# Kernel tuning notes

Hardware: AMD Instinct MI355X
Metric: run time of the kernel (lower is better)

## Reference

```python
import jax, jax.numpy as jnp
import numpy as np

B, S, H = 2, 2048, 2048
NH, NKV, HD = 16, 4, 128  # heads, kv heads, head_dim
GROUP = NH // NKV
THETA = 10000.0
NEG = -1e9


def _rope_tables(seq_len, head_dim, theta):
    inv_freq = 1.0 / (theta ** (jnp.arange(0, head_dim, 2, dtype=jnp.float32) / head_dim))
    t = jnp.arange(seq_len, dtype=jnp.float32)
    freqs = jnp.outer(t, inv_freq)                 # [S, HD/2]
    emb = jnp.concatenate([freqs, freqs], axis=-1)  # [S, HD]
    return jnp.cos(emb), jnp.sin(emb)


def _rotate_half(x):
    half = x.shape[-1] // 2
    return jnp.concatenate([-x[..., half:], x[..., :half]], axis=-1)


def setup_inputs() -> dict:
    key = jax.random.key(0)
    ks = jax.random.split(key, 5)
    scale = 0.02
    x = jax.random.normal(ks[0], (B, S, H), dtype=jnp.float32)
    Wq = jax.random.normal(ks[1], (NH * HD, H), dtype=jnp.float32) * scale
    Wk = jax.random.normal(ks[2], (NKV * HD, H), dtype=jnp.float32) * scale
    Wv = jax.random.normal(ks[3], (NKV * HD, H), dtype=jnp.float32) * scale
    Wo = jax.random.normal(ks[4], (H, NH * HD), dtype=jnp.float32) * scale
    cos, sin = _rope_tables(S, HD, THETA)
    # additive causal mask: 0 on/below diagonal, -1e9 above
    causal = jnp.triu(jnp.full((S, S), NEG, dtype=jnp.float32), k=1)
    mask = causal[None, None]  # [1,1,S,S]
    return {"x": x, "Wq": Wq, "Wk": Wk, "Wv": Wv, "Wo": Wo,
            "cos": cos, "sin": sin, "mask": mask}


def reference(x, Wq, Wk, Wv, Wo, cos, sin, mask):
    b, s, _ = x.shape
    # projections (nn.Linear, no bias): y = x @ W.T
    q = (x @ Wq.T).reshape(b, s, NH, HD).transpose(0, 2, 1, 3)    # [B,NH,S,D]
    k = (x @ Wk.T).reshape(b, s, NKV, HD).transpose(0, 2, 1, 3)   # [B,NKV,S,D]
    v = (x @ Wv.T).reshape(b, s, NKV, HD).transpose(0, 2, 1, 3)   # [B,NKV,S,D]
    # RoPE
    c = cos[None, None]  # [1,1,S,D]
    sn = sin[None, None]
    q = q * c + _rotate_half(q) * sn
    k = k * c + _rotate_half(k) * sn
    # GQA: repeat KV heads to match query heads (mirrors _repeat_kv)
    k = jnp.repeat(k, GROUP, axis=1)  # [B,NH,S,D]
    v = jnp.repeat(v, GROUP, axis=1)
    # scaled dot-product attention with additive mask
    scores = jnp.einsum('bhqd,bhkd->bhqk', q, k) / jnp.sqrt(jnp.float32(HD))
    scores = scores + mask
    p = jax.nn.softmax(scores, axis=-1)
    ctx = jnp.einsum('bhqk,bhkd->bhqd', p, v)            # [B,NH,S,D]
    ctx = ctx.transpose(0, 2, 1, 3).reshape(b, s, NH * HD)
    return ctx @ Wo.T
```

## Files before the change

### kernel.cpp

```cpp
#include <hip/hip_runtime.h>
#include <stdint.h>

#define B_   2
#define S_   2048
#define H_   2048
#define NH_  16
#define NKV_ 4
#define HD_  128
#define M_   (B_ * S_)

typedef short bf16x8 __attribute__((ext_vector_type(8)));
typedef float f32x4  __attribute__((ext_vector_type(4)));

__device__ __forceinline__ float b2f(unsigned short u) {
  union { unsigned int u; float f; } v; v.u = ((unsigned int)u) << 16; return v.f;
}
__device__ __forceinline__ unsigned short f2b(float f) {
  union { float f; unsigned int u; } v; v.f = f;
  unsigned int u = v.u;
  unsigned int r = (u + 0x7FFFu + ((u >> 16) & 1u)) >> 16;
  return (unsigned short)r;
}
__device__ __forceinline__ uint4 pack8(const float4& a, const float4& b) {
  uint4 r;
  r.x = (unsigned)f2b(a.x) | ((unsigned)f2b(a.y) << 16);
  r.y = (unsigned)f2b(a.z) | ((unsigned)f2b(a.w) << 16);
  r.z = (unsigned)f2b(b.x) | ((unsigned)f2b(b.y) << 16);
  r.w = (unsigned)f2b(b.z) | ((unsigned)f2b(b.w) << 16);
  return r;
}
__device__ __forceinline__ void gload_lds(const unsigned short* g, unsigned short* l) {
  __builtin_amdgcn_global_load_lds(
      (const __attribute__((address_space(1))) unsigned int*)g,
      (__attribute__((address_space(3))) unsigned int*)l, 16, 0, 0);
}

__global__ void cvt_bf16(const float* __restrict__ src, unsigned short* __restrict__ dst, int n8)
{
  int i = blockIdx.x * blockDim.x + threadIdx.x;
  if (i >= n8) return;
  const float* p = src + (size_t)i * 8;
  uint4 v = pack8(*reinterpret_cast<const float4*>(p), *reinterpret_cast<const float4*>(p + 4));
  *reinterpret_cast<uint4*>(dst + (size_t)i * 8) = v;
}

template<bool CF32>
__global__ __launch_bounds__(256, 4) void gemm_ld(
    const unsigned short* __restrict__ A, const unsigned short* __restrict__ B0,
    const unsigned short* __restrict__ B1, void* __restrict__ C0, void* __restrict__ C1,
    int N, int K, int nxHalf)
{
  __shared__ unsigned short As[128 * 64];
  __shared__ unsigned short Bs[128 * 64];

  const unsigned short* Bm; void* Cm; int colBase;
  if ((int)blockIdx.x < nxHalf) { Bm = B0; Cm = C0; colBase = blockIdx.x * 128; }
  else                          { Bm = B1; Cm = C1; colBase = (blockIdx.x - nxHalf) * 128; }
  const int rowBase = blockIdx.y * 128;

  const int tid    = threadIdx.x;
  const int lane   = tid & 63;
  const int wid    = tid >> 6;
  const int wrow   = wid >> 1;
  const int wcol   = wid & 1;
  const int lane15 = lane & 15;
  const int quad   = lane >> 4;

  const f32x4 zero = {0.f, 0.f, 0.f, 0.f};
  f32x4 acc[4][4];
#pragma unroll
  for (int i = 0; i < 4; i++)
#pragma unroll
    for (int j = 0; j < 4; j++) acc[i][j] = zero;

  const int lr  = lane >> 3;
  const int sc8 = (lane & 7) ^ lr;

  for (int kb = 0; kb < K; kb += 64) {
    __syncthreads();
#pragma unroll
    for (int i = 0; i < 4; i++) {
      const int rg = (i * 4 + wid) * 8;
      const int r  = rg + lr;
      gload_lds(A  + (size_t)(rowBase + r) * K + kb + sc8 * 8, As + rg * 64);
      gload_lds(Bm + (size_t)(colBase + r) * K + kb + sc8 * 8, Bs + rg * 64);
    }
    __syncthreads();
#pragma unroll
    for (int kc = 0; kc < 2; kc++) {
      bf16x8 af[4], bf[4];
#pragma unroll
      for (int g = 0; g < 4; g++) {
        const int ra = wrow * 64 + g * 16 + lane15;
        const int rb = wcol * 64 + g * 16 + lane15;
        af[g] = *reinterpret_cast<const bf16x8*>(As + ra * 64 + (((kc * 4 + quad) ^ (ra & 7)) * 8));
        bf[g] = *reinterpret_cast<const bf16x8*>(Bs + rb * 64 + (((kc * 4 + quad) ^ (rb & 7)) * 8));
      }
#pragma unroll
      for (int i = 0; i < 4; i++)
#pragma unroll
        for (int j = 0; j < 4; j++)
          acc[i][j] = __builtin_amdgcn_mfma_f32_16x16x32_bf16(af[i], bf[j], acc[i][j], 0, 0, 0);
    }
  }

  if (CF32) {
    float* Cf = (float*)Cm;
#pragma unroll
    for (int i = 0; i < 4; i++) {
      int row = rowBase + wrow * 64 + i * 16 + quad * 4;
#pragma unroll
      for (int j = 0; j < 4; j++) {
        int col = colBase + wcol * 64 + j * 16 + lane15;
#pragma unroll
        for (int rr = 0; rr < 4; rr++)
          Cf[(size_t)(row + rr) * N + col] = acc[i][j][rr];
      }
    }
  } else {
    unsigned short* Cb = (unsigned short*)Cm;
#pragma unroll
    for (int i = 0; i < 4; i++) {
      int row = rowBase + wrow * 64 + i * 16 + quad * 4;
#pragma unroll
      for (int j = 0; j < 4; j++) {
        int col = colBase + wcol * 64 + j * 16 + lane15;
#pragma unroll
        for (int rr = 0; rr < 4; rr++)
          Cb[(size_t)(row + rr) * N + col] = f2b(acc[i][j][rr]);
      }
    }
  }
}

template<bool OPROJ>
__global__ __launch_bounds__(256, 3) void gemm_k(
    const void* __restrict__ A, const float* __restrict__ B0, const float* __restrict__ B1,
    void* __restrict__ C0, void* __restrict__ C1, int N, int K, int nxHalf)
{
  __shared__ unsigned short As[128 * 72];
  __shared__ unsigned short Bs[128 * 72];

  const float* Bm; void* Cm; int colBase;
  if ((int)blockIdx.x < nxHalf) { Bm = B0; Cm = C0; colBase = blockIdx.x * 128; }
  else                          { Bm = B1; Cm = C1; colBase = (blockIdx.x - nxHalf) * 128; }
  const int rowBase = blockIdx.y * 128;

  const int tid    = threadIdx.x;
  const int lane   = tid & 63;
  const int wid    = tid >> 6;
  const int wrow   = wid >> 1;
  const int wcol   = wid & 1;
  const int lane15 = lane & 15;
  const int quad   = lane >> 4;

  const f32x4 zero = {0.f, 0.f, 0.f, 0.f};
  f32x4 acc[4][4];
#pragma unroll
  for (int i = 0; i < 4; i++)
#pragma unroll
    for (int j = 0; j < 4; j++) acc[i][j] = zero;

  const int r0 = tid >> 3;
  const int c8 = tid & 7;

  uint4 av[4], bv[4];
#pragma unroll
  for (int p = 0; p < 4; p++) {
    int r = r0 + 32 * p;
    if (OPROJ) {
      av[p] = *reinterpret_cast<const uint4*>((const unsigned short*)A + (size_t)(rowBase + r) * K + c8 * 8);
    } else {
      const float* pA = (const float*)A + (size_t)(rowBase + r) * K + c8 * 8;
      av[p] = pack8(*reinterpret_cast<const float4*>(pA), *reinterpret_cast<const float4*>(pA + 4));
    }
    const float* pB = Bm + (size_t)(colBase + r) * K + c8 * 8;
    bv[p] = pack8(*reinterpret_cast<const float4*>(pB), *reinterpret_cast<const float4*>(pB + 4));
  }

  for (int kb = 0; kb < K; kb += 64) {
    __syncthreads();
#pragma unroll
    for (int p = 0; p < 4; p++) {
      int r = r0 + 32 * p;
      *reinterpret_cast<uint4*>(As + r * 72 + c8 * 8) = av[p];
      *reinterpret_cast<uint4*>(Bs + r * 72 + c8 * 8) = bv[p];
    }
    __syncthreads();
    const int kn = kb + 64;
    if (kn < K) {
#pragma unroll
      for (int p = 0; p < 4; p++) {
        int r = r0 + 32 * p;
        if (OPROJ) {
          av[p] = *reinterpret_cast<const uint4*>((const unsigned short*)A + (size_t)(rowBase + r) * K + kn + c8 * 8);
        } else {
          const float* pA = (const float*)A + (size_t)(rowBase + r) * K + kn + c8 * 8;
          av[p] = pack8(*reinterpret_cast<const float4*>(pA), *reinterpret_cast<const float4*>(pA + 4));
        }
        const float* pB = Bm + (size_t)(colBase + r) * K + kn + c8 * 8;
        bv[p] = pack8(*reinterpret_cast<const float4*>(pB), *reinterpret_cast<const float4*>(pB + 4));
      }
    }
#pragma unroll
    for (int kc = 0; kc < 2; kc++) {
      bf16x8 af[4], bf[4];
#pragma unroll
      for (int g = 0; g < 4; g++) {
        af[g] = *reinterpret_cast<const bf16x8*>(As + (wrow * 64 + g * 16 + lane15) * 72 + kc * 32 + quad * 8);
        bf[g] = *reinterpret_cast<const bf16x8*>(Bs + (wcol * 64 + g * 16 + lane15) * 72 + kc * 32 + quad * 8);
      }
#pragma unroll
      for (int i = 0; i < 4; i++)
#pragma unroll
        for (int j = 0; j < 4; j++)
          acc[i][j] = __builtin_amdgcn_mfma_f32_16x16x32_bf16(af[i], bf[j], acc[i][j], 0, 0, 0);
    }
  }

  if (OPROJ) {
    float* Cf = (float*)Cm;
#pragma unroll
    for (int i = 0; i < 4; i++) {
      int row = rowBase + wrow * 64 + i * 16 + quad * 4;
#pragma unroll
      for (int j = 0; j < 4; j++) {
        int col = colBase + wcol * 64 + j * 16 + lane15;
#pragma unroll
        for (int rr = 0; rr < 4; rr++)
          Cf[(size_t)(row + rr) * N + col] = acc[i][j][rr];
      }
    }
  } else {
    unsigned short* Cb = (unsigned short*)Cm;
#pragma unroll
    for (int i = 0; i < 4; i++) {
      int row = rowBase + wrow * 64 + i * 16 + quad * 4;
#pragma unroll
      for (int j = 0; j < 4; j++) {
        int col = colBase + wcol * 64 + j * 16 + lane15;
#pragma unroll
        for (int rr = 0; rr < 4; rr++)
          Cb[(size_t)(row + rr) * N + col] = f2b(acc[i][j][rr]);
      }
    }
  }
}

__global__ void rope_k(unsigned short* __restrict__ Qb, unsigned short* __restrict__ Kb,
                       const float* __restrict__ cosT, const float* __restrict__ sinT)
{
  const int per_tok = (NH_ + NKV_) * 64;
  int idx = blockIdx.x * blockDim.x + threadIdx.x;
  int t = idx / per_tok;
  int r = idx - t * per_tok;
  if (t >= M_) return;
  int s = t & (S_ - 1);
  unsigned short* base;
  int d;
  if (r < NH_ * 64) {
    int h = r >> 6; d = r & 63;
    base = Qb + (size_t)t * (NH_ * HD_) + h * HD_ + d;
  } else {
    int rk = r - NH_ * 64;
    int h = rk >> 6; d = rk & 63;
    base = Kb + (size_t)t * (NKV_ * HD_) + h * HD_ + d;
  }
  float c  = cosT[s * HD_ + d];
  float sn = sinT[s * HD_ + d];
  float x0 = b2f(base[0]);
  float x1 = b2f(base[64]);
  base[0]  = f2b(x0 * c - x1 * sn);
  base[64] = f2b(x1 * c + x0 * sn);
}

__global__ void transp_v(const unsigned short* __restrict__ Vb, unsigned short* __restrict__ VT)
{
  __shared__ unsigned short Ls[64 * 72];
  const int t0 = blockIdx.x * 64;
  const int d0 = blockIdx.y * 64;
  const int tid = threadIdx.x;
  const int r = tid >> 3, c = tid & 7;
#pragma unroll
  for (int p = 0; p < 2; p++)
    *reinterpret_cast<uint4*>(Ls + (r + 32 * p) * 72 + c * 8) =
      *reinterpret_cast<const uint4*>(Vb + (size_t)(t0 + r + 32 * p) * (NKV_ * HD_) + d0 + c * 8);
  __syncthreads();
  const int bq = t0 >> 11, s0 = t0 & (S_ - 1);
#pragma unroll
  for (int p = 0; p < 2; p++) {
    int dl = r + 32 * p;
    unsigned short tmp[8];
#pragma unroll
    for (int j = 0; j < 8; j++) tmp[j] = Ls[(c * 8 + j) * 72 + dl];
    *reinterpret_cast<uint4*>(VT + (size_t)(bq * 512 + d0 + dl) * S_ + s0 + c * 8) =
      *reinterpret_cast<uint4*>(tmp);
  }
}

__global__ __launch_bounds__(512, 2) void attn(
    const unsigned short* Q, const unsigned short* __restrict__ Kc,
    const unsigned short* __restrict__ VT, unsigned short* O)
{
  __shared__ unsigned short Ks[64 * 136];
  __shared__ unsigned short Vs[128 * 72];
  __shared__ unsigned short Ps[8 * 16 * 72];

  const int tid    = threadIdx.x;
  const int lane   = tid & 63;
  const int w      = tid >> 6;
  const int lane15 = lane & 15;
  const int quad   = lane >> 4;
  const int p      = blockIdx.x & 15;
  const int half   = blockIdx.x >> 4;
  const int kvh    = blockIdx.y;
  const int b      = blockIdx.z;
  const int hloc   = w >> 1;
  const int strip  = w & 1;
  const int h      = kvh * 4 + hloc;
  const size_t bS  = (size_t)b * S_;

  const int qt1 = 31 - p;
  const int qt2 = p;
  const int nkt1 = qt1 + 1;
  const int nkt2 = qt2 + 1;
  const int ntot = nkt1 + nkt2;
  const int qb1 = qt1 * 64 + half * 32;
  const int qb2 = qt2 * 64 + half * 32;

  unsigned short* Psw = Ps + w * (16 * 72);

  const int skr = tid >> 4;
  const int skc = tid & 15;
  const int svd = tid >> 3;
  const int svc = tid & 7;
  const unsigned short* Kbase = Kc + bS * (NKV_ * HD_) + kvh * HD_;
  const unsigned short* Vbase = VT + (size_t)(b * 512 + kvh * HD_) * S_;

  const f32x4 zero = {0.f, 0.f, 0.f, 0.f};
  f32x4 ctx[8];
#pragma unroll
  for (int ng = 0; ng < 8; ng++) ctx[ng] = zero;
  float l_i[4] = {0.f, 0.f, 0.f, 0.f};

  bf16x8 qf[4];
  {
    const unsigned short* qp = Q + (bS + qb1 + strip * 16 + lane15) * (NH_ * HD_) + h * HD_ + quad * 8;
#pragma unroll
    for (int kc = 0; kc < 4; kc++) qf[kc] = *reinterpret_cast<const bf16x8*>(qp + kc * 32);
  }

  uint4 kreg[2], vreg[2];
#pragma unroll
  for (int p2 = 0; p2 < 2; p2++) {
    kreg[p2] = *reinterpret_cast<const uint4*>(Kbase + (size_t)(skr + 32 * p2) * (NKV_ * HD_) + skc * 8);
    vreg[p2] = *reinterpret_cast<const uint4*>(Vbase + (size_t)(svd + 64 * p2) * S_ + svc * 8);
  }

  const float scale = 0.08838834764831845f;

  for (int seq = 0; seq < ntot; seq++) {
    const bool ph1 = (seq < nkt1);
    const int kt   = ph1 ? seq : seq - nkt1;
    const int nkt  = ph1 ? nkt1 : nkt2;
    const int qb   = ph1 ? qb1 : qb2;

    __syncthreads();
#pragma unroll
    for (int p2 = 0; p2 < 2; p2++) {
      *reinterpret_cast<uint4*>(Ks + (skr + 32 * p2) * 136 + skc * 8) = kreg[p2];
      *reinterpret_cast<uint4*>(Vs + (svd + 64 * p2) * 72 + svc * 8) = vreg[p2];
    }
    __syncthreads();

    if (seq + 1 < ntot) {
      const int ktn  = (seq + 1 < nkt1) ? seq + 1 : seq + 1 - nkt1;
      const int key0 = ktn * 64;
#pragma unroll
      for (int p2 = 0; p2 < 2; p2++) {
        kreg[p2] = *reinterpret_cast<const uint4*>(Kbase + (size_t)(key0 + skr + 32 * p2) * (NKV_ * HD_) + skc * 8);
        vreg[p2] = *reinterpret_cast<const uint4*>(Vbase + (size_t)(svd + 64 * p2) * S_ + key0 + svc * 8);
      }
    }

    f32x4 sc[4];
#pragma unroll
    for (int cg = 0; cg < 4; cg++) sc[cg] = zero;
#pragma unroll
    for (int cg = 0; cg < 4; cg++)
#pragma unroll
      for (int kc = 0; kc < 4; kc++) {
        bf16x8 kf = *reinterpret_cast<const bf16x8*>(Ks + (cg * 16 + lane15) * 136 + kc * 32 + quad * 8);
        sc[cg] = __builtin_amdgcn_mfma_f32_16x16x32_bf16(qf[kc], kf, sc[cg], 0, 0, 0);
      }

    if (kt == nkt - 1) {
#pragma unroll
      for (int cg = 0; cg < 4; cg++) {
        int key = kt * 64 + cg * 16 + lane15;
#pragma unroll
        for (int rr = 0; rr < 4; rr++) {
          int qrow = qb + strip * 16 + quad * 4 + rr;
          float v = sc[cg][rr] * scale;
          sc[cg][rr] = (key <= qrow) ? v : -1.0e9f;
        }
      }
    } else {
#pragma unroll
      for (int cg = 0; cg < 4; cg++)
#pragma unroll
        for (int rr = 0; rr < 4; rr++) sc[cg][rr] *= scale;
    }

#pragma unroll
    for (int rr = 0; rr < 4; rr++) {
      float p0 = __expf(sc[0][rr]);
      float p1 = __expf(sc[1][rr]);
      float p2 = __expf(sc[2][rr]);
      float p3 = __expf(sc[3][rr]);
      l_i[rr] += (p0 + p1) + (p2 + p3);
      int prow = (quad * 4 + rr) * 72;
      Psw[prow + lane15]      = f2b(p0);
      Psw[prow + 16 + lane15] = f2b(p1);
      Psw[prow + 32 + lane15] = f2b(p2);
      Psw[prow + 48 + lane15] = f2b(p3);
    }
    __threadfence_block();

    bf16x8 pf[2];
#pragma unroll
    for (int kc = 0; kc < 2; kc++)
      pf[kc] = *reinterpret_cast<const bf16x8*>(&Psw[lane15 * 72 + kc * 32 + quad * 8]);

#pragma unroll
    for (int ng = 0; ng < 8; ng++)
#pragma unroll
      for (int kc = 0; kc < 2; kc++) {
        bf16x8 vf = *reinterpret_cast<const bf16x8*>(Vs + (ng * 16 + lane15) * 72 + kc * 32 + quad * 8);
        ctx[ng] = __builtin_amdgcn_mfma_f32_16x16x32_bf16(pf[kc], vf, ctx[ng], 0, 0, 0);
      }

    if (kt == nkt - 1) {
      float inv[4];
#pragma unroll
      for (int rr = 0; rr < 4; rr++) {
        float l = l_i[rr];
        l += __shfl_xor(l, 1);
        l += __shfl_xor(l, 2);
        l += __shfl_xor(l, 4);
        l += __shfl_xor(l, 8);
        inv[rr] = 1.0f / l;
      }
      const int qrow = qb + strip * 16 + quad * 4;
#pragma unroll
      for (int ng = 0; ng < 8; ng++)
#pragma unroll
        for (int rr = 0; rr < 4; rr++)
          O[(bS + qrow + rr) * (NH_ * HD_) + h * HD_ + ng * 16 + lane15] = f2b(ctx[ng][rr] * inv[rr]);

      if (seq + 1 < ntot) {
        const unsigned short* qp = Q + (bS + qb2 + strip * 16 + lane15) * (NH_ * HD_) + h * HD_ + quad * 8;
#pragma unroll
        for (int kc = 0; kc < 4; kc++) qf[kc] = *reinterpret_cast<const bf16x8*>(qp + kc * 32);
#pragma unroll
        for (int ng = 0; ng < 8; ng++) ctx[ng] = zero;
#pragma unroll
        for (int rr = 0; rr < 4; rr++) l_i[rr] = 0.f;
      }
    }
  }
}

extern "C" void kernel_launch(void* const* d_in, const int* in_sizes, int n_in,
                              void* d_out, int out_size, void* d_ws, size_t ws_size,
                              hipStream_t stream) {
  const float* x    = (const float*)d_in[0];
  const float* Wq   = (const float*)d_in[1];
  const float* Wk   = (const float*)d_in[2];
  const float* Wv   = (const float*)d_in[3];
  const float* Wo   = (const float*)d_in[4];
  const float* cosT = (const float*)d_in[5];
  const float* sinT = (const float*)d_in[6];
  float* out = (float*)d_out;

  const size_t qElems  = (size_t)M_ * NH_ * HD_;
  const size_t xElems  = (size_t)M_ * H_;
  const size_t wqElems = (size_t)H_ * H_;
  const size_t wkElems = (size_t)NKV_ * HD_ * H_;
  const size_t bigNeed = (qElems + xElems + 2 * wqElems + 2 * wkElems) * 2 + 256;

  if (ws_size < qElems * 2 + 256) return;

  unsigned short* Qb = (unsigned short*)d_ws;
  unsigned short* Kb = (unsigned short*)d_out;
  unsigned short* Vb = Kb + (size_t)M_ * NKV_ * HD_;
  unsigned short* VT = Vb + (size_t)M_ * NKV_ * HD_;

  dim3 blk(256);
  const int rope_threads = M_ * (NH_ + NKV_) * 64;

  if (ws_size >= bigNeed) {
    unsigned short* xb  = Qb + qElems;
    unsigned short* Wqb = xb + xElems;
    unsigned short* Wob = Wqb + wqElems;
    unsigned short* Wkb = Wob + wqElems;
    unsigned short* Wvb = Wkb + wkElems;

    cvt_bf16<<<dim3((int)(xElems / 8 + 255) / 256), blk, 0, stream>>>(x,  xb,  (int)(xElems / 8));
    cvt_bf16<<<dim3((int)(wqElems / 8 + 255) / 256), blk, 0, stream>>>(Wq, Wqb, (int)(wqElems / 8));
    cvt_bf16<<<dim3((int)(wkElems / 8 + 255) / 256), blk, 0, stream>>>(Wk, Wkb, (int)(wkElems / 8));
    cvt_bf16<<<dim3((int)(wkElems / 8 + 255) / 256), blk, 0, stream>>>(Wv, Wvb, (int)(wkElems / 8));
    cvt_bf16<<<dim3((int)(wqElems / 8 + 255) / 256), blk, 0, stream>>>(Wo, Wob, (int)(wqElems / 8));

    gemm_ld<false><<<dim3(16, 32), blk, 0, stream>>>(xb, Wqb, Wqb, Qb, Qb, NH_ * HD_, H_, 16);
    gemm_ld<false><<<dim3(8, 32), blk, 0, stream>>>(xb, Wkb, Wvb, Kb, Vb, NKV_ * HD_, H_, 4);

    rope_k<<<dim3((rope_threads + 255) / 256), blk, 0, stream>>>(Qb, Kb, cosT, sinT);
    transp_v<<<dim3(M_ / 64, (NKV_ * HD_) / 64), blk, 0, stream>>>(Vb, VT);
    attn<<<dim3(32, NKV_, B_), dim3(512), 0, stream>>>(Qb, Kb, VT, Qb);

    gemm_ld<true><<<dim3(16, 32), blk, 0, stream>>>(Qb, Wob, Wob, out, out, H_, NH_ * HD_, 16);
  } else {
    gemm_k<false><<<dim3(16, 32), blk, 0, stream>>>(x, Wq, Wq, Qb, Qb, NH_ * HD_, H_, 16);
    gemm_k<false><<<dim3(8, 32), blk, 0, stream>>>(x, Wk, Wv, Kb, Vb, NKV_ * HD_, H_, 4);

    rope_k<<<dim3((rope_threads + 255) / 256), blk, 0, stream>>>(Qb, Kb, cosT, sinT);
    transp_v<<<dim3(M_ / 64, (NKV_ * HD_) / 64), blk, 0, stream>>>(Vb, VT);
    attn<<<dim3(32, NKV_, B_), dim3(512), 0, stream>>>(Qb, Kb, VT, Qb);

    gemm_k<true><<<dim3(16, 32), blk, 0, stream>>>(Qb, Wo, Wo, out, out, H_, NH_ * HD_, 16);
  }
}
```

Baseline: 387.4 us.

## Restructure attention around 32x32 MFMA with register-resident P and swizzled LDS

Rewrites the attention kernel to use 32x32x16 bf16 MFMA and computes scores transposed (K times Q). The probabilities then stay in registers and are rearranged with v_permlane32_swap, removing the per-wave LDS round trip for P. K and V tiles are stored in LDS with an XOR swizzle instead of padding, to avoid bank conflicts. Each block now handles one 64-row query tile instead of a balanced pair of 32-row half tiles, so the cost is uneven per-block work across the causal triangle.

```diff
diff --git a/kernel.cpp b/kernel.cpp
--- a/kernel.cpp
+++ b/kernel.cpp
@@ -11,6 +11,7 @@
 
 typedef short bf16x8 __attribute__((ext_vector_type(8)));
 typedef float f32x4  __attribute__((ext_vector_type(4)));
+typedef float f32x16 __attribute__((ext_vector_type(16)));
 
 __device__ __forceinline__ float b2f(unsigned short u) {
   union { unsigned int u; float f; } v; v.u = ((unsigned int)u) << 16; return v.f;
@@ -299,174 +300,148 @@
 }
 
 __global__ __launch_bounds__(512, 2) void attn(
-    const unsigned short* Q, const unsigned short* __restrict__ Kc,
-    const unsigned short* __restrict__ VT, unsigned short* O)
+    const unsigned short* __restrict__ Q, const unsigned short* __restrict__ Kc,
+    const unsigned short* __restrict__ VT, unsigned short* __restrict__ O)
 {
-  __shared__ unsigned short Ks[64 * 136];
-  __shared__ unsigned short Vs[128 * 72];
-  __shared__ unsigned short Ps[8 * 16 * 72];
-
-  const int tid    = threadIdx.x;
-  const int lane   = tid & 63;
-  const int w      = tid >> 6;
-  const int lane15 = lane & 15;
-  const int quad   = lane >> 4;
-  const int p      = blockIdx.x & 15;
-  const int half   = blockIdx.x >> 4;
-  const int kvh    = blockIdx.y;
-  const int b      = blockIdx.z;
-  const int hloc   = w >> 1;
-  const int strip  = w & 1;
-  const int h      = kvh * 4 + hloc;
-  const size_t bS  = (size_t)b * S_;
-
-  const int qt1 = 31 - p;
-  const int qt2 = p;
-  const int nkt1 = qt1 + 1;
-  const int nkt2 = qt2 + 1;
-  const int ntot = nkt1 + nkt2;
-  const int qb1 = qt1 * 64 + half * 32;
-  const int qb2 = qt2 * 64 + half * 32;
-
-  unsigned short* Psw = Ps + w * (16 * 72);
-
-  const int skr = tid >> 4;
-  const int skc = tid & 15;
-  const int svd = tid >> 3;
-  const int svc = tid & 7;
+  __shared__ unsigned short Ks[64 * 128];
+  __shared__ unsigned short Vs[128 * 64];
+  __shared__ float Ll[8 * 32];
+
+  const int tid  = threadIdx.x;
+  const int lane = tid & 63;
+  const int w    = tid >> 6;
+  const int l31  = lane & 31;
+  const int hi   = lane >> 5;
+  const int qt   = blockIdx.x;
+  const int kvh  = blockIdx.y;
+  const int b    = blockIdx.z;
+  const int h    = kvh * 4 + (w & 3);
+  const int rg   = w >> 2;
+  const size_t bS = (size_t)b * S_;
+  const int ntot = qt + 1;
+
+  const int kr   = tid >> 4;
+  const int kc16 = tid & 15;
+  const int vd   = tid >> 3;
+  const int vc8  = tid & 7;
+
   const unsigned short* Kbase = Kc + bS * (NKV_ * HD_) + kvh * HD_;
   const unsigned short* Vbase = VT + (size_t)(b * 512 + kvh * HD_) * S_;
 
-  const f32x4 zero = {0.f, 0.f, 0.f, 0.f};
-  f32x4 ctx[8];
-#pragma unroll
-  for (int ng = 0; ng < 8; ng++) ctx[ng] = zero;
-  float l_i[4] = {0.f, 0.f, 0.f, 0.f};
-
-  bf16x8 qf[4];
+  bf16x8 qf[8];
   {
-    const unsigned short* qp = Q + (bS + qb1 + strip * 16 + lane15) * (NH_ * HD_) + h * HD_ + quad * 8;
-#pragma unroll
-    for (int kc = 0; kc < 4; kc++) qf[kc] = *reinterpret_cast<const bf16x8*>(qp + kc * 32);
-  }
+    const unsigned short* qp = Q + (bS + qt * 64 + rg * 32 + l31) * (NH_ * HD_) + h * HD_ + hi * 8;
+#pragma unroll
+    for (int kc = 0; kc < 8; kc++) qf[kc] = *reinterpret_cast<const bf16x8*>(qp + kc * 16);
+  }
+
+  f32x16 ctx[4];
+#pragma unroll
+  for (int ng = 0; ng < 4; ng++)
+#pragma unroll
+    for (int r = 0; r < 16; r++) ctx[ng][r] = 0.f;
+  float lsum = 0.f;
 
   uint4 kreg[2], vreg[2];
 #pragma unroll
   for (int p2 = 0; p2 < 2; p2++) {
-    kreg[p2] = *reinterpret_cast<const uint4*>(Kbase + (size_t)(skr + 32 * p2) * (NKV_ * HD_) + skc * 8);
-    vreg[p2] = *reinterpret_cast<const uint4*>(Vbase + (size_t)(svd + 64 * p2) * S_ + svc * 8);
+    kreg[p2] = *reinterpret_cast<const uint4*>(Kbase + (size_t)(kr + 32 * p2) * (NKV_ * HD_) + kc16 * 8);
+    vreg[p2] = *reinterpret_cast<const uint4*>(Vbase + (size_t)(vd + 64 * p2) * S_ + vc8 * 8);
   }
 
   const float scale = 0.08838834764831845f;
 
-  for (int seq = 0; seq < ntot; seq++) {
-    const bool ph1 = (seq < nkt1);
-    const int kt   = ph1 ? seq : seq - nkt1;
-    const int nkt  = ph1 ? nkt1 : nkt2;
-    const int qb   = ph1 ? qb1 : qb2;
-
+  for (int kt = 0; kt < ntot; kt++) {
     __syncthreads();
 #pragma unroll
     for (int p2 = 0; p2 < 2; p2++) {
-      *reinterpret_cast<uint4*>(Ks + (skr + 32 * p2) * 136 + skc * 8) = kreg[p2];
-      *reinterpret_cast<uint4*>(Vs + (svd + 64 * p2) * 72 + svc * 8) = vreg[p2];
+      const int row = kr + 32 * p2;
+      *reinterpret_cast<uint4*>(Ks + row * 128 + ((kc16 ^ (row & 15)) * 8)) = kreg[p2];
+      const int d = vd + 64 * p2;
+      *reinterpret_cast<uint4*>(Vs + d * 64 + ((vc8 ^ (d & 7)) * 8)) = vreg[p2];
     }
     __syncthreads();
 
-    if (seq + 1 < ntot) {
-      const int ktn  = (seq + 1 < nkt1) ? seq + 1 : seq + 1 - nkt1;
-      const int key0 = ktn * 64;
+    if (kt + 1 < ntot) {
+      const int key0 = (kt + 1) * 64;
 #pragma unroll
       for (int p2 = 0; p2 < 2; p2++) {
-        kreg[p2] = *reinterpret_cast<const uint4*>(Kbase + (size_t)(key0 + skr + 32 * p2) * (NKV_ * HD_) + skc * 8);
-        vreg[p2] = *reinterpret_cast<const uint4*>(Vbase + (size_t)(svd + 64 * p2) * S_ + key0 + svc * 8);
-      }
-    }
-
-    f32x4 sc[4];
-#pragma unroll
-    for (int cg = 0; cg < 4; cg++) sc[cg] = zero;
-#pragma unroll
-    for (int cg = 0; cg < 4; cg++)
+        kreg[p2] = *reinterpret_cast<const uint4*>(Kbase + (size_t)(key0 + kr + 32 * p2) * (NKV_ * HD_) + kc16 * 8);
+        vreg[p2] = *reinterpret_cast<const uint4*>(Vbase + (size_t)(vd + 64 * p2) * S_ + key0 + vc8 * 8);
+      }
+    }
+
+    f32x16 sc0, sc1;
+#pragma unroll
+    for (int r = 0; r < 16; r++) { sc0[r] = 0.f; sc1[r] = 0.f; }
+#pragma unroll
+    for (int kc = 0; kc < 8; kc++) {
+      const int ch = ((kc * 2 + hi) ^ (l31 & 15)) * 8;
+      bf16x8 kf0 = *reinterpret_cast<const bf16x8*>(Ks + l31 * 128 + ch);
+      sc0 = __builtin_amdgcn_mfma_f32_32x32x16_bf16(kf0, qf[kc], sc0, 0, 0, 0);
+      bf16x8 kf1 = *reinterpret_cast<const bf16x8*>(Ks + (32 + l31) * 128 + ch);
+      sc1 = __builtin_amdgcn_mfma_f32_32x32x16_bf16(kf1, qf[kc], sc1, 0, 0, 0);
+    }
+
+    const int lim = (kt == qt) ? (rg * 32 + l31) : 4096;
+    bf16x8 pfrag[4];
+#pragma unroll
+    for (int cg = 0; cg < 2; cg++) {
+      float pe[16];
+#pragma unroll
+      for (int r = 0; r < 16; r++) {
+        float v = (cg ? sc1[r] : sc0[r]) * scale;
+        const int kp = cg * 32 + (r & 3) + 8 * (r >> 2) + 4 * hi;
+        v = (kp <= lim) ? v : -1.0e9f;
+        float e = __expf(v);
+        pe[r] = e;
+        lsum += e;
+      }
+      unsigned wd[8];
+#pragma unroll
+      for (int j = 0; j < 8; j++) {
+        unsigned t;
+        asm("v_cvt_pk_bf16_f32 %0, %1, %2" : "=v"(t) : "v"(pe[2 * j]), "v"(pe[2 * j + 1]));
+        wd[j] = t;
+      }
+      asm("v_permlane32_swap_b32 %0, %1" : "+v"(wd[0]), "+v"(wd[2]));
+      asm("v_permlane32_swap_b32 %0, %1" : "+v"(wd[1]), "+v"(wd[3]));
+      asm("v_permlane32_swap_b32 %0, %1" : "+v"(wd[4]), "+v"(wd[6]));
+      asm("v_permlane32_swap_b32 %0, %1" : "+v"(wd[5]), "+v"(wd[7]));
+      union { unsigned u[4]; bf16x8 v8; } ua, ub;
+      ua.u[0] = wd[0]; ua.u[1] = wd[1]; ua.u[2] = wd[2]; ua.u[3] = wd[3];
+      ub.u[0] = wd[4]; ub.u[1] = wd[5]; ub.u[2] = wd[6]; ub.u[3] = wd[7];
+      pfrag[cg * 2]     = ua.v8;
+      pfrag[cg * 2 + 1] = ub.v8;
+    }
+
+#pragma unroll
+    for (int ng = 0; ng < 4; ng++) {
+      const int drow = ng * 32 + l31;
 #pragma unroll
       for (int kc = 0; kc < 4; kc++) {
-        bf16x8 kf = *reinterpret_cast<const bf16x8*>(Ks + (cg * 16 + lane15) * 136 + kc * 32 + quad * 8);
-        sc[cg] = __builtin_amdgcn_mfma_f32_16x16x32_bf16(qf[kc], kf, sc[cg], 0, 0, 0);
-      }
-
-    if (kt == nkt - 1) {
-#pragma unroll
-      for (int cg = 0; cg < 4; cg++) {
-        int key = kt * 64 + cg * 16 + lane15;
-#pragma unroll
-        for (int rr = 0; rr < 4; rr++) {
-          int qrow = qb + strip * 16 + quad * 4 + rr;
-          float v = sc[cg][rr] * scale;
-          sc[cg][rr] = (key <= qrow) ? v : -1.0e9f;
-        }
-      }
-    } else {
-#pragma unroll
-      for (int cg = 0; cg < 4; cg++)
-#pragma unroll
-        for (int rr = 0; rr < 4; rr++) sc[cg][rr] *= scale;
-    }
-
-#pragma unroll
-    for (int rr = 0; rr < 4; rr++) {
-      float p0 = __expf(sc[0][rr]);
-      float p1 = __expf(sc[1][rr]);
-      float p2 = __expf(sc[2][rr]);
-      float p3 = __expf(sc[3][rr]);
-      l_i[rr] += (p0 + p1) + (p2 + p3);
-      int prow = (quad * 4 + rr) * 72;
-      Psw[prow + lane15]      = f2b(p0);
-      Psw[prow + 16 + lane15] = f2b(p1);
-      Psw[prow + 32 + lane15] = f2b(p2);
-      Psw[prow + 48 + lane15] = f2b(p3);
-    }
-    __threadfence_block();
-
-    bf16x8 pf[2];
-#pragma unroll
-    for (int kc = 0; kc < 2; kc++)
-      pf[kc] = *reinterpret_cast<const bf16x8*>(&Psw[lane15 * 72 + kc * 32 + quad * 8]);
-
-#pragma unroll
-    for (int ng = 0; ng < 8; ng++)
-#pragma unroll
-      for (int kc = 0; kc < 2; kc++) {
-        bf16x8 vf = *reinterpret_cast<const bf16x8*>(Vs + (ng * 16 + lane15) * 72 + kc * 32 + quad * 8);
-        ctx[ng] = __builtin_amdgcn_mfma_f32_16x16x32_bf16(pf[kc], vf, ctx[ng], 0, 0, 0);
-      }
-
-    if (kt == nkt - 1) {
-      float inv[4];
-#pragma unroll
-      for (int rr = 0; rr < 4; rr++) {
-        float l = l_i[rr];
-        l += __shfl_xor(l, 1);
-        l += __shfl_xor(l, 2);
-        l += __shfl_xor(l, 4);
-        l += __shfl_xor(l, 8);
-        inv[rr] = 1.0f / l;
-      }
-      const int qrow = qb + strip * 16 + quad * 4;
-#pragma unroll
-      for (int ng = 0; ng < 8; ng++)
-#pragma unroll
-        for (int rr = 0; rr < 4; rr++)
-          O[(bS + qrow + rr) * (NH_ * HD_) + h * HD_ + ng * 16 + lane15] = f2b(ctx[ng][rr] * inv[rr]);
-
-      if (seq + 1 < ntot) {
-        const unsigned short* qp = Q + (bS + qb2 + strip * 16 + lane15) * (NH_ * HD_) + h * HD_ + quad * 8;
-#pragma unroll
-        for (int kc = 0; kc < 4; kc++) qf[kc] = *reinterpret_cast<const bf16x8*>(qp + kc * 32);
-#pragma unroll
-        for (int ng = 0; ng < 8; ng++) ctx[ng] = zero;
-#pragma unroll
-        for (int rr = 0; rr < 4; rr++) l_i[rr] = 0.f;
-      }
+        bf16x8 vf = *reinterpret_cast<const bf16x8*>(Vs + drow * 64 + (((kc * 2 + hi) ^ (l31 & 7)) * 8));
+        ctx[ng] = __builtin_amdgcn_mfma_f32_32x32x16_bf16(pfrag[kc], vf, ctx[ng], 0, 0, 0);
+      }
+    }
+  }
+
+  {
+    float lt = lsum + __shfl_xor(lsum, 32);
+    Ll[w * 32 + l31] = 1.0f / lt;
+  }
+  f32x4 iv[4];
+#pragma unroll
+  for (int g = 0; g < 4; g++)
+    iv[g] = *reinterpret_cast<const f32x4*>(&Ll[w * 32 + 4 * hi + 8 * g]);
+
+  const size_t orow0 = bS + qt * 64 + rg * 32;
+#pragma unroll
+  for (int ng = 0; ng < 4; ng++) {
+#pragma unroll
+    for (int r = 0; r < 16; r++) {
+      const int qp = (r & 3) + 8 * (r >> 2) + 4 * hi;
+      O[(orow0 + qp) * (NH_ * HD_) + h * HD_ + ng * 32 + l31] = f2b(ctx[ng][r] * iv[r >> 2][r & 3]);
     }
   }
 }
```

Measured after the change: 394.0 us. About the same (+1.7%).
